# Performance work log

Hardware: AMD Instinct MI355X
Metric: run time of the kernel (lower is better)

Reference implementation:

```python
import jax, jax.numpy as jnp
import numpy as np

OUT_F, IN_F = 4096, 4096
N_FREQ = 10000
SCALING = 150.0


def iwht(x):
    """Unnormalized fast Walsh-Hadamard transform along axis 0. x: [n, m], n power of 2."""
    n, m = x.shape
    steps = int(np.log2(n))
    x = x.reshape((2,) * steps + (m,))
    for ax in range(steps):  # log2(n) butterfly stages
        a, b = jnp.split(x, 2, axis=ax)
        x = jnp.concatenate([a + b, a - b], axis=ax)
    return x.reshape(n, m)


def setup_inputs() -> dict:
    key = jax.random.key(0)
    k1, k2, k3, k4 = jax.random.split(key, 4)
    x = jax.random.normal(k1, (2, 512, IN_F), dtype=jnp.float32)
    weight = jax.random.normal(k2, (OUT_F, IN_F), dtype=jnp.float32) * 0.02
    spectrum = jax.random.normal(k3, (N_FREQ,), dtype=jnp.float32)
    indices = jax.random.randint(k4, (2, N_FREQ), 0, OUT_F, dtype=jnp.int64)
    return {"x": x, "weight": weight, "spectrum": spectrum, "indices": indices}


def reference(x, weight, spectrum, indices):
    out_f, in_f = weight.shape
    # sparse scatter of spectrum into dense (out, in) matrix
    dense = jnp.zeros((out_f, in_f), dtype=spectrum.dtype).at[indices[0], indices[1]].set(spectrum)
    # inverse WHT along out axis, scaled
    delta_w = iwht(dense) * (SCALING / np.sqrt(np.float32(out_f)))
    # F.linear(x, base_w + delta_w)
    return jnp.einsum('bsi,oi->bso', x, weight + delta_w.astype(x.dtype))
```

## Files before the change

### kernel.cpp

```cpp
#include <hip/hip_runtime.h>

typedef unsigned short ushort_t;

#define M_DIM 1024
#define N_DIM 4096
#define K_DIM 4096
#define NFREQ 10000
constexpr float SCALE = 150.0f / 64.0f;

typedef __bf16 bf16x8_t  __attribute__((ext_vector_type(8)));
typedef float  f32x16_t  __attribute__((ext_vector_type(16)));

__device__ inline ushort_t f2bf(float f) {
  union { __bf16 h; ushort_t u; } v;
  v.h = (__bf16)f;
  return v.u;
}

__global__ __launch_bounds__(256) void build_w4(
    const float* __restrict__ weight,
    const float* __restrict__ spectrum,
    const int* __restrict__ idx,
    const float* __restrict__ x,
    ushort_t* __restrict__ wb,
    ushort_t* __restrict__ xb) {
  if (blockIdx.y == 0) {
    int flat = blockIdx.x * 256 + threadIdx.x;
#pragma unroll 4
    for (int k = 0; k < 64; ++k) {
      int i = flat + k * 16384;
      float4 v = ((const float4*)x)[i];
      ushort4 o;
      o.x = f2bf(v.x); o.y = f2bf(v.y); o.z = f2bf(v.z); o.w = f2bf(v.w);
      ((ushort4*)xb)[i] = o;
    }
    return;
  }

  constexpr int CAP = 1024;
  __shared__ unsigned e_raw[CAP];
  __shared__ float    v_raw[CAP];
  __shared__ uint2    ev_srt[CAP];
  __shared__ int cnt;
  __shared__ int cstart[65];
  __shared__ int coff[64];
  __shared__ int ccnt[64];
  __shared__ unsigned walsh16[16];

  const int tid = threadIdx.x;
  const int ci0 = blockIdx.x * 64;
  const int o0  = (blockIdx.y - 1) * 256;

  if (tid == 0) cnt = 0;
  if (tid < 64) ccnt[tid] = 0;
  if (tid < 16) {
    unsigned m = tid;
    unsigned w = (m & 1 ? 0xAAAAu : 0u) ^ (m & 2 ? 0xCCCCu : 0u)
               ^ (m & 4 ? 0xF0F0u : 0u) ^ (m & 8 ? 0xFF00u : 0u);
    walsh16[m] = w;
  }
  __syncthreads();

  for (int j = tid; j < NFREQ; j += 256) {
    int c = idx[NFREQ + j];
    if ((c >> 6) == (int)blockIdx.x) {
      int p = atomicAdd(&cnt, 1);
      if (p < CAP) {
        e_raw[p] = ((unsigned)(c & 63) << 26) | ((unsigned)j << 12) | (unsigned)idx[j];
        v_raw[p] = spectrum[j];
        atomicAdd(&ccnt[c & 63], 1);
      }
    }
  }
  __syncthreads();
  const int n = cnt < CAP ? cnt : CAP;

  if (tid < 64) {
    int v = ccnt[tid];
    int s = v;
    for (int d = 1; d < 64; d <<= 1) {
      int o = __shfl_up(s, d, 64);
      if (tid >= d) s += o;
    }
    cstart[tid + 1] = s;
    if (tid == 0) cstart[0] = 0;
    coff[tid] = s - v;
  }
  __syncthreads();
  for (int e = tid; e < n; e += 256) {
    unsigned w = e_raw[e];
    int dc = w >> 26;
    int p = atomicAdd(&coff[dc], 1);
    ev_srt[p] = make_uint2(w, __float_as_uint(v_raw[e]));
  }
  __syncthreads();

  for (int e = tid; e < n; e += 256) {
    uint2 ev = ev_srt[e];
    int dc = ev.x >> 26;
    unsigned r = ev.x & 0xFFFu, j = (ev.x >> 12) & 0x3FFFu;
    int s0 = cstart[dc], e0 = cstart[dc + 1];
    bool dead = false;
    for (int p = s0; p < e0; ++p) {
      unsigned w2 = ev_srt[p].x;
      if ((w2 & 0xFFFu) == r && ((w2 >> 12) & 0x3FFFu) > j) dead = true;
    }
    if (dead) ev_srt[e].y = 0u;
  }
  __syncthreads();

  const int dc0   = (tid & 15) * 4;
  const int rof   = tid >> 4;
  const int obase = o0 + rof * 16;

  float acc[4][16];
#pragma unroll
  for (int c = 0; c < 4; ++c)
#pragma unroll
    for (int j = 0; j < 16; ++j) acc[c][j] = 0.0f;

#pragma unroll
  for (int c = 0; c < 4; ++c) {
    const int s = cstart[dc0 + c], e = cstart[dc0 + c + 1];
    for (int p = s; p < e; ++p) {
      uint2 ev = ev_srt[p];
      unsigned r = ev.x & 0xFFFu;
      unsigned W = walsh16[r & 15u];
      unsigned sx = ev.y ^ ((unsigned)(__popc(obase & r) & 1) << 31);
#pragma unroll
      for (int j = 0; j < 16; ++j) {
        acc[c][j] += __uint_as_float(sx ^ ((W << (31 - j)) & 0x80000000u));
      }
    }
  }

  size_t g = (size_t)obase * K_DIM + ci0 + dc0;
#pragma unroll
  for (int j = 0; j < 16; ++j) {
    float4 w4 = *(const float4*)&weight[g];
    ushort4 ov;
    ov.x = f2bf(w4.x + SCALE * acc[0][j]);
    ov.y = f2bf(w4.y + SCALE * acc[1][j]);
    ov.z = f2bf(w4.z + SCALE * acc[2][j]);
    ov.w = f2bf(w4.w + SCALE * acc[3][j]);
    *(ushort4*)&wb[g] = ov;
    g += K_DIM;
  }
}

__global__ __launch_bounds__(256) void gemm_bt(
    const ushort_t* __restrict__ A,
    const ushort_t* __restrict__ B,
    float* __restrict__ C0,
    float* __restrict__ C1,
    int klen) {
  constexpr int BM = 128, BN = 128, BK = 64;
  __shared__ __align__(16) ushort_t As[BM * BK];
  __shared__ __align__(16) ushort_t Bs[BN * BK];

  const int tid  = threadIdx.x;
  const int wave = tid >> 6, lane = tid & 63;
  const int wrow = wave >> 1, wcol = wave & 1;
  const int l32  = lane & 31, half = lane >> 5;

  const int fid = blockIdx.y * 32 + blockIdx.x;
  const int xcd = fid & 7, w8 = fid >> 3;
  const int sx = w8 & 7, sy = w8 >> 3;
  const int cx = xcd & 3, cy = xcd >> 2;
  const int bn = (cx * 8 + sx) * BN;
  const int bm = (cy * 4 + sy) * BM;

  const int kbeg = blockIdx.z * klen;
  float* __restrict__ dst = blockIdx.z == 0
      ? C0 : C1 + (size_t)(blockIdx.z - 1) * M_DIM * N_DIM;

  const int srow8 = lane >> 3;
  const int sq    = lane & 7;

  f32x16_t acc[2][2] = {};

  for (int kt = kbeg; kt < kbeg + klen; kt += BK) {
#pragma unroll
    for (int c = 0; c < 4; ++c) {
      int ch = wave * 4 + c;
      int gr = ch * 8 + srow8;
      int qg = sq ^ (gr & 7);
      const ushort_t* ga = A + (size_t)(bm + gr) * K_DIM + kt + qg * 8;
      __builtin_amdgcn_global_load_lds(
          (const __attribute__((address_space(1))) void*)ga,
          (__attribute__((address_space(3))) void*)&As[ch * 512], 16, 0, 0);
      const ushort_t* gb = B + (size_t)(bn + gr) * K_DIM + kt + qg * 8;
      __builtin_amdgcn_global_load_lds(
          (const __attribute__((address_space(1))) void*)gb,
          (__attribute__((address_space(3))) void*)&Bs[ch * 512], 16, 0, 0);
    }
    __syncthreads();

    bf16x8_t af[2][4], bfr[2][4];
#pragma unroll
    for (int mi = 0; mi < 2; ++mi) {
#pragma unroll
      for (int h = 0; h < 4; ++h) {
        int q = h * 2 + half;
        int ar = wrow * 64 + mi * 32 + l32;
        af[mi][h]  = *(const bf16x8_t*)&As[ar * BK + ((q ^ (ar & 7)) * 8)];
        int br = wcol * 64 + mi * 32 + l32;
        bfr[mi][h] = *(const bf16x8_t*)&Bs[br * BK + ((q ^ (br & 7)) * 8)];
      }
    }
#pragma unroll
    for (int h = 0; h < 4; ++h)
#pragma unroll
      for (int mi = 0; mi < 2; ++mi)
#pragma unroll
        for (int nj = 0; nj < 2; ++nj)
          acc[mi][nj] = __builtin_amdgcn_mfma_f32_32x32x16_bf16(
              af[mi][h], bfr[nj][h], acc[mi][nj], 0, 0, 0);
    __syncthreads();
  }

#pragma unroll
  for (int mi = 0; mi < 2; ++mi) {
#pragma unroll
    for (int nj = 0; nj < 2; ++nj) {
      int col  = bn + wcol * 64 + nj * 32 + l32;
      int rwb  = bm + wrow * 64 + mi * 32 + 4 * half;
#pragma unroll
      for (int reg = 0; reg < 16; ++reg) {
        int row = rwb + (reg & 3) + 8 * (reg >> 2);
        dst[(size_t)row * N_DIM + col] = acc[mi][nj][reg];
      }
    }
  }
}

__global__ __launch_bounds__(256) void reduce_n(float* __restrict__ out,
                                                const float* __restrict__ part,
                                                int npart) {
  int i = blockIdx.x * 256 + threadIdx.x;
  float4 a = ((const float4*)out)[i];
  for (int t = 0; t < npart; ++t) {
    float4 b = ((const float4*)(part + (size_t)t * M_DIM * N_DIM))[i];
    a.x += b.x; a.y += b.y; a.z += b.z; a.w += b.w;
  }
  ((float4*)out)[i] = a;
}

extern "C" void kernel_launch(void* const* d_in, const int* in_sizes, int n_in,
                              void* d_out, int out_size, void* d_ws, size_t ws_size,
                              hipStream_t stream) {
  const float* x        = (const float*)d_in[0];
  const float* weight   = (const float*)d_in[1];
  const float* spectrum = (const float*)d_in[2];
  const int*   indices  = (const int*)d_in[3];
  float* out = (float*)d_out;

  char* ws = (char*)d_ws;
  const size_t WB_BYTES = (size_t)N_DIM * K_DIM * 2;
  const size_t XB_BYTES = (size_t)M_DIM * K_DIM * 2;
  const size_t P1_BYTES = (size_t)M_DIM * N_DIM * 4;

  ushort_t* wb = (ushort_t*)ws;
  ushort_t* xb = (ushort_t*)(ws + WB_BYTES);
  float* part = (float*)(ws + WB_BYTES + XB_BYTES);

  int zsplit = (ws_size >= WB_BYTES + XB_BYTES + P1_BYTES) ? 2 : 1;

  build_w4<<<dim3(64, 17), 256, 0, stream>>>(weight, spectrum, indices, x, wb, xb);

  gemm_bt<<<dim3(N_DIM / 128, M_DIM / 128, zsplit), 256, 0, stream>>>(
      xb, wb, out, part, K_DIM / zsplit);
  if (zsplit > 1)
    reduce_n<<<(M_DIM * N_DIM / 4) / 256, 256, 0, stream>>>(out, part, zsplit - 1);
}
```

Before: 185.8 us.

## Triple-buffer GEMM LDS loads with async prefetch and larger 128x256 tiles

Replaces the single-buffered bf16 GEMM with a 3-stage LDS pipeline. Global-to-LDS loads for tile t+2 are issued while tile t is computed, and the per-tile syncthreads pairs become a vmcnt wait plus one barrier. The block tile grows to 128x256 with 512 threads (8 waves), the XCD-aware tile mapping is adjusted, and MFMA sections get raised wave priority. This aims to hide global load latency behind MFMA work. The cost is much more LDS per block (144KB), which limits occupancy, and fewer blocks (128 per z-slice) on a large CU count.

```diff
diff --git a/kernel.cpp b/kernel.cpp
--- a/kernel.cpp
+++ b/kernel.cpp
@@ -148,66 +148,101 @@
   }
 }
 
-__global__ __launch_bounds__(256) void gemm_bt(
+__global__ __launch_bounds__(512) void gemm_pipe(
     const ushort_t* __restrict__ A,
     const ushort_t* __restrict__ B,
     float* __restrict__ C0,
     float* __restrict__ C1,
     int klen) {
-  constexpr int BM = 128, BN = 128, BK = 64;
-  __shared__ __align__(16) ushort_t As[BM * BK];
-  __shared__ __align__(16) ushort_t Bs[BN * BK];
+  constexpr int BM = 128, BN = 256, BK = 64;
+  constexpr int A_US = BM * BK;
+  constexpr int B_US = BN * BK;
+  __shared__ __align__(16) ushort_t lds[3 * (A_US + B_US)];
 
   const int tid  = threadIdx.x;
   const int wave = tid >> 6, lane = tid & 63;
-  const int wrow = wave >> 1, wcol = wave & 1;
+  const int wrow = wave >> 2;
+  const int wcol = wave & 3;
   const int l32  = lane & 31, half = lane >> 5;
 
-  const int fid = blockIdx.y * 32 + blockIdx.x;
-  const int xcd = fid & 7, w8 = fid >> 3;
-  const int sx = w8 & 7, sy = w8 >> 3;
-  const int cx = xcd & 3, cy = xcd >> 2;
-  const int bn = (cx * 8 + sx) * BN;
-  const int bm = (cy * 4 + sy) * BM;
+  const int fid = blockIdx.y * 16 + blockIdx.x;
+  const int xcd = fid & 7, w16 = fid >> 3;
+  const int bn = ((xcd & 3) * 4 + (w16 & 3)) * BN;
+  const int bm = ((xcd >> 2) * 4 + (w16 >> 2)) * BM;
 
   const int kbeg = blockIdx.z * klen;
+  const int nt   = klen / BK;
   float* __restrict__ dst = blockIdx.z == 0
       ? C0 : C1 + (size_t)(blockIdx.z - 1) * M_DIM * N_DIM;
 
-  const int srow8 = lane >> 3;
-  const int sq    = lane & 7;
+  auto stage = [&](int tt, int p) {
+    const int kt = kbeg + tt * BK;
+    ushort_t* abase = lds + p * A_US;
+    ushort_t* bbase = lds + 3 * A_US + p * B_US;
+#pragma unroll
+    for (int l = 0; l < 6; ++l) {
+      int s  = tid + l * 512;
+      int sb = (tid & ~63) + l * 512;
+      if (l < 2) {
+        int gr = s >> 3, qg = (s & 7) ^ (gr & 7);
+        const ushort_t* ga = A + (size_t)(bm + gr) * K_DIM + kt + qg * 8;
+        __builtin_amdgcn_global_load_lds(
+            (const __attribute__((address_space(1))) void*)ga,
+            (__attribute__((address_space(3))) void*)(abase + sb * 8), 16, 0, 0);
+      } else {
+        int s2 = s - 1024;
+        int gr = s2 >> 3, qg = (s2 & 7) ^ (gr & 7);
+        const ushort_t* gb = B + (size_t)(bn + gr) * K_DIM + kt + qg * 8;
+        __builtin_amdgcn_global_load_lds(
+            (const __attribute__((address_space(1))) void*)gb,
+            (__attribute__((address_space(3))) void*)(bbase + (sb - 1024) * 8), 16, 0, 0);
+      }
+    }
+  };
 
   f32x16_t acc[2][2] = {};
 
-  for (int kt = kbeg; kt < kbeg + klen; kt += BK) {
-#pragma unroll
-    for (int c = 0; c < 4; ++c) {
-      int ch = wave * 4 + c;
-      int gr = ch * 8 + srow8;
-      int qg = sq ^ (gr & 7);
-      const ushort_t* ga = A + (size_t)(bm + gr) * K_DIM + kt + qg * 8;
-      __builtin_amdgcn_global_load_lds(
-          (const __attribute__((address_space(1))) void*)ga,
-          (__attribute__((address_space(3))) void*)&As[ch * 512], 16, 0, 0);
-      const ushort_t* gb = B + (size_t)(bn + gr) * K_DIM + kt + qg * 8;
-      __builtin_amdgcn_global_load_lds(
-          (const __attribute__((address_space(1))) void*)gb,
-          (__attribute__((address_space(3))) void*)&Bs[ch * 512], 16, 0, 0);
-    }
-    __syncthreads();
+  stage(0, 0);
+  if (nt > 1) {
+    stage(1, 1);
+    __builtin_amdgcn_sched_barrier(0);
+    asm volatile("s_waitcnt vmcnt(6)" ::: "memory");
+  } else {
+    __builtin_amdgcn_sched_barrier(0);
+    asm volatile("s_waitcnt vmcnt(0)" ::: "memory");
+  }
+  __builtin_amdgcn_sched_barrier(0);
+  __builtin_amdgcn_s_barrier();
+  __builtin_amdgcn_sched_barrier(0);
+
+  for (int t = 0; t < nt; ++t) {
+    const int cb = t % 3;
+    const ushort_t* as_ = lds + cb * A_US;
+    const ushort_t* bs_ = lds + 3 * A_US + cb * B_US;
+
+    if (t + 2 < nt) stage(t + 2, (t + 2) % 3);
 
     bf16x8_t af[2][4], bfr[2][4];
 #pragma unroll
     for (int mi = 0; mi < 2; ++mi) {
+      int ar = wrow * 64 + mi * 32 + l32;
 #pragma unroll
       for (int h = 0; h < 4; ++h) {
         int q = h * 2 + half;
-        int ar = wrow * 64 + mi * 32 + l32;
-        af[mi][h]  = *(const bf16x8_t*)&As[ar * BK + ((q ^ (ar & 7)) * 8)];
-        int br = wcol * 64 + mi * 32 + l32;
-        bfr[mi][h] = *(const bf16x8_t*)&Bs[br * BK + ((q ^ (br & 7)) * 8)];
-      }
-    }
+        af[mi][h] = *(const bf16x8_t*)&as_[ar * BK + ((q ^ (ar & 7)) * 8)];
+      }
+    }
+#pragma unroll
+    for (int nj = 0; nj < 2; ++nj) {
+      int br = wcol * 64 + nj * 32 + l32;
+#pragma unroll
+      for (int h = 0; h < 4; ++h) {
+        int q = h * 2 + half;
+        bfr[nj][h] = *(const bf16x8_t*)&bs_[br * BK + ((q ^ (br & 7)) * 8)];
+      }
+    }
+
+    __builtin_amdgcn_s_setprio(1);
 #pragma unroll
     for (int h = 0; h < 4; ++h)
 #pragma unroll
@@ -216,7 +251,21 @@
         for (int nj = 0; nj < 2; ++nj)
           acc[mi][nj] = __builtin_amdgcn_mfma_f32_32x32x16_bf16(
               af[mi][h], bfr[nj][h], acc[mi][nj], 0, 0, 0);
-    __syncthreads();
+    __builtin_amdgcn_s_setprio(0);
+
+    if (t + 2 < nt) {
+      __builtin_amdgcn_sched_barrier(0);
+      asm volatile("s_waitcnt vmcnt(6)" ::: "memory");
+      __builtin_amdgcn_sched_barrier(0);
+      __builtin_amdgcn_s_barrier();
+      __builtin_amdgcn_sched_barrier(0);
+    } else if (t + 1 < nt) {
+      __builtin_amdgcn_sched_barrier(0);
+      asm volatile("s_waitcnt vmcnt(0)" ::: "memory");
+      __builtin_amdgcn_sched_barrier(0);
+      __builtin_amdgcn_s_barrier();
+      __builtin_amdgcn_sched_barrier(0);
+    }
   }
 
 #pragma unroll
@@ -268,7 +317,7 @@
 
   build_w4<<<dim3(64, 17), 256, 0, stream>>>(weight, spectrum, indices, x, wb, xb);
 
-  gemm_bt<<<dim3(N_DIM / 128, M_DIM / 128, zsplit), 256, 0, stream>>>(
+  gemm_pipe<<<dim3(N_DIM / 256, M_DIM / 128, zsplit), 512, 0, stream>>>(
       xb, wb, out, part, K_DIM / zsplit);
   if (zsplit > 1)
     reduce_n<<<(M_DIM * N_DIM / 4) / 256, 256, 0, stream>>>(out, part, zsplit - 1);
```

Measured after the change: 186.4 us. No clear change (+0.3%).

## Fuse split-K reduction into GEMM epilogue via per-tile tickets and ready flags

Applied to the files above, without the earlier changes.

Drops the separate reduce kernel. Each output tile's two split-K blocks take a ticket. The first writes its partial to the workspace and raises a ready flag, and the second spins on that flag and writes the summed result to out. Build_w4 resets the flags each launch. This removes a kernel launch and one full read-modify-write pass over out, at the cost of a spin-wait. The spin-wait can deadlock if the second-arriving block is resident while its partner is not scheduled, and it can stall waves.

```diff
diff --git a/kernel.cpp b/kernel.cpp
--- a/kernel.cpp
+++ b/kernel.cpp
@@ -23,9 +23,17 @@
     const int* __restrict__ idx,
     const float* __restrict__ x,
     ushort_t* __restrict__ wb,
-    ushort_t* __restrict__ xb) {
+    ushort_t* __restrict__ xb,
+    int* __restrict__ tickets,
+    int* __restrict__ ready) {
   if (blockIdx.y == 0) {
     int flat = blockIdx.x * 256 + threadIdx.x;
+    if (blockIdx.x == 0) {
+      __hip_atomic_store(&tickets[threadIdx.x], 0,
+                         __ATOMIC_RELAXED, __HIP_MEMORY_SCOPE_AGENT);
+      __hip_atomic_store(&ready[threadIdx.x], 0,
+                         __ATOMIC_RELAXED, __HIP_MEMORY_SCOPE_AGENT);
+    }
 #pragma unroll 4
     for (int k = 0; k < 64; ++k) {
       int i = flat + k * 16384;
@@ -151,12 +159,15 @@
 __global__ __launch_bounds__(256) void gemm_bt(
     const ushort_t* __restrict__ A,
     const ushort_t* __restrict__ B,
-    float* __restrict__ C0,
-    float* __restrict__ C1,
+    float* __restrict__ out,
+    float* __restrict__ part,
+    int* __restrict__ tickets,
+    int* __restrict__ ready,
     int klen) {
   constexpr int BM = 128, BN = 128, BK = 64;
   __shared__ __align__(16) ushort_t As[BM * BK];
   __shared__ __align__(16) ushort_t Bs[BN * BK];
+  __shared__ int tkt_s;
 
   const int tid  = threadIdx.x;
   const int wave = tid >> 6, lane = tid & 63;
@@ -171,8 +182,6 @@
   const int bm = (cy * 4 + sy) * BM;
 
   const int kbeg = blockIdx.z * klen;
-  float* __restrict__ dst = blockIdx.z == 0
-      ? C0 : C1 + (size_t)(blockIdx.z - 1) * M_DIM * N_DIM;
 
   const int srow8 = lane >> 3;
   const int sq    = lane & 7;
@@ -219,31 +228,65 @@
     __syncthreads();
   }
 
-#pragma unroll
-  for (int mi = 0; mi < 2; ++mi) {
-#pragma unroll
-    for (int nj = 0; nj < 2; ++nj) {
-      int col  = bn + wcol * 64 + nj * 32 + l32;
-      int rwb  = bm + wrow * 64 + mi * 32 + 4 * half;
-#pragma unroll
-      for (int reg = 0; reg < 16; ++reg) {
-        int row = rwb + (reg & 3) + 8 * (reg >> 2);
-        dst[(size_t)row * N_DIM + col] = acc[mi][nj][reg];
-      }
-    }
-  }
-}
-
-__global__ __launch_bounds__(256) void reduce_n(float* __restrict__ out,
-                                                const float* __restrict__ part,
-                                                int npart) {
-  int i = blockIdx.x * 256 + threadIdx.x;
-  float4 a = ((const float4*)out)[i];
-  for (int t = 0; t < npart; ++t) {
-    float4 b = ((const float4*)(part + (size_t)t * M_DIM * N_DIM))[i];
-    a.x += b.x; a.y += b.y; a.z += b.z; a.w += b.w;
-  }
-  ((float4*)out)[i] = a;
+  if (gridDim.z == 1) {
+#pragma unroll
+    for (int mi = 0; mi < 2; ++mi)
+#pragma unroll
+      for (int nj = 0; nj < 2; ++nj) {
+        int col  = bn + wcol * 64 + nj * 32 + l32;
+        int rwb  = bm + wrow * 64 + mi * 32 + 4 * half;
+#pragma unroll
+        for (int reg = 0; reg < 16; ++reg) {
+          int row = rwb + (reg & 3) + 8 * (reg >> 2);
+          out[(size_t)row * N_DIM + col] = acc[mi][nj][reg];
+        }
+      }
+    return;
+  }
+
+  if (tid == 0) tkt_s = atomicAdd(&tickets[fid], 1);
+  __syncthreads();
+  const bool first = (tkt_s == 0);
+
+  if (first) {
+#pragma unroll
+    for (int mi = 0; mi < 2; ++mi)
+#pragma unroll
+      for (int nj = 0; nj < 2; ++nj) {
+        int col  = bn + wcol * 64 + nj * 32 + l32;
+        int rwb  = bm + wrow * 64 + mi * 32 + 4 * half;
+#pragma unroll
+        for (int reg = 0; reg < 16; ++reg) {
+          int row = rwb + (reg & 3) + 8 * (reg >> 2);
+          part[(size_t)row * N_DIM + col] = acc[mi][nj][reg];
+        }
+      }
+    __threadfence();
+    __syncthreads();
+    if (tid == 0)
+      __hip_atomic_store(&ready[fid], 1, __ATOMIC_RELEASE,
+                         __HIP_MEMORY_SCOPE_AGENT);
+  } else {
+    if (tid == 0) {
+      while (__hip_atomic_load(&ready[fid], __ATOMIC_ACQUIRE,
+                               __HIP_MEMORY_SCOPE_AGENT) == 0)
+        __builtin_amdgcn_s_sleep(1);
+    }
+    __syncthreads();
+#pragma unroll
+    for (int mi = 0; mi < 2; ++mi)
+#pragma unroll
+      for (int nj = 0; nj < 2; ++nj) {
+        int col  = bn + wcol * 64 + nj * 32 + l32;
+        int rwb  = bm + wrow * 64 + mi * 32 + 4 * half;
+#pragma unroll
+        for (int reg = 0; reg < 16; ++reg) {
+          int row = rwb + (reg & 3) + 8 * (reg >> 2);
+          size_t o = (size_t)row * N_DIM + col;
+          out[o] = part[o] + acc[mi][nj][reg];
+        }
+      }
+  }
 }
 
 extern "C" void kernel_launch(void* const* d_in, const int* in_sizes, int n_in,
@@ -259,17 +302,20 @@
   const size_t WB_BYTES = (size_t)N_DIM * K_DIM * 2;
   const size_t XB_BYTES = (size_t)M_DIM * K_DIM * 2;
   const size_t P1_BYTES = (size_t)M_DIM * N_DIM * 4;
+  const size_t FLAG_BYTES = 2 * 256 * sizeof(int);
 
   ushort_t* wb = (ushort_t*)ws;
   ushort_t* xb = (ushort_t*)(ws + WB_BYTES);
-  float* part = (float*)(ws + WB_BYTES + XB_BYTES);
-
-  int zsplit = (ws_size >= WB_BYTES + XB_BYTES + P1_BYTES) ? 2 : 1;
-
-  build_w4<<<dim3(64, 17), 256, 0, stream>>>(weight, spectrum, indices, x, wb, xb);
+  float* part  = (float*)(ws + WB_BYTES + XB_BYTES);
+  int* tickets = (int*)(ws + WB_BYTES + XB_BYTES + P1_BYTES);
+  int* ready   = tickets + 256;
+
+  int zsplit =
+      (ws_size >= WB_BYTES + XB_BYTES + P1_BYTES + FLAG_BYTES) ? 2 : 1;
+
+  build_w4<<<dim3(64, 17), 256, 0, stream>>>(weight, spectrum, indices, x,
+                                             wb, xb, tickets, ready);
 
   gemm_bt<<<dim3(N_DIM / 128, M_DIM / 128, zsplit), 256, 0, stream>>>(
-      xb, wb, out, part, K_DIM / zsplit);
-  if (zsplit > 1)
-    reduce_n<<<(M_DIM * N_DIM / 4) / 256, 256, 0, stream>>>(out, part, zsplit - 1);
+      xb, wb, out, part, tickets, ready, K_DIM / zsplit);
 }
```

Result: slower. 222.3 us (+19.6%).

## Apply sparse Walsh delta to activations instead of materializing dense delta weight

Applied to the files above, without the earlier changes.

Instead of building W + iWHT(delta) densely, the weight is just converted to bf16, and the sparse spectrum contribution is applied per output row: each block scatters spectrum*x into a 4096-vector in shared memory and runs an in-LDS Walsh-Hadamard transform, then adds it to the GEMM result. The split-K reduction is fused into this step. It removes the dense per-element Walsh accumulation from weight building, at the cost of 1024 blocks each doing an LDS WHT and shared-memory atomics, and it keeps the delta in fp32 instead of rounding it into bf16 weights.

```diff
diff --git a/kernel.cpp b/kernel.cpp
--- a/kernel.cpp
+++ b/kernel.cpp
@@ -17,26 +17,15 @@
   return v.u;
 }
 
-__global__ __launch_bounds__(256) void build_w4(
+__global__ __launch_bounds__(256) void prep_cvt(
     const float* __restrict__ weight,
+    const float* __restrict__ x,
     const float* __restrict__ spectrum,
     const int* __restrict__ idx,
-    const float* __restrict__ x,
-    ushort_t* __restrict__ wb,
-    ushort_t* __restrict__ xb) {
-  if (blockIdx.y == 0) {
-    int flat = blockIdx.x * 256 + threadIdx.x;
-#pragma unroll 4
-    for (int k = 0; k < 64; ++k) {
-      int i = flat + k * 16384;
-      float4 v = ((const float4*)x)[i];
-      ushort4 o;
-      o.x = f2bf(v.x); o.y = f2bf(v.y); o.z = f2bf(v.z); o.w = f2bf(v.w);
-      ((ushort4*)xb)[i] = o;
-    }
-    return;
-  }
-
+    ushort_t* __restrict__ wbb,
+    ushort_t* __restrict__ xb,
+    uint2* __restrict__ ent,
+    int* __restrict__ cst) {
   constexpr int CAP = 1024;
   __shared__ unsigned e_raw[CAP];
   __shared__ float    v_raw[CAP];
@@ -45,25 +34,38 @@
   __shared__ int cstart[65];
   __shared__ int coff[64];
   __shared__ int ccnt[64];
-  __shared__ unsigned walsh16[16];
 
   const int tid = threadIdx.x;
-  const int ci0 = blockIdx.x * 64;
-  const int o0  = (blockIdx.y - 1) * 256;
-
+
+  if (blockIdx.x >= 64) {
+    const int i0 = (blockIdx.x - 64) * 256 + tid;
+#pragma unroll
+    for (int k = 0; k < 8; ++k) {
+      int i = i0 + k * 524288;
+      float4 v = ((const float4*)weight)[i];
+      ushort4 o;
+      o.x = f2bf(v.x); o.y = f2bf(v.y); o.z = f2bf(v.z); o.w = f2bf(v.w);
+      ((ushort4*)wbb)[i] = o;
+    }
+#pragma unroll
+    for (int k = 0; k < 2; ++k) {
+      int i = i0 + k * 524288;
+      float4 v = ((const float4*)x)[i];
+      ushort4 o;
+      o.x = f2bf(v.x); o.y = f2bf(v.y); o.z = f2bf(v.z); o.w = f2bf(v.w);
+      ((ushort4*)xb)[i] = o;
+    }
+    return;
+  }
+
+  const int g = blockIdx.x;
   if (tid == 0) cnt = 0;
   if (tid < 64) ccnt[tid] = 0;
-  if (tid < 16) {
-    unsigned m = tid;
-    unsigned w = (m & 1 ? 0xAAAAu : 0u) ^ (m & 2 ? 0xCCCCu : 0u)
-               ^ (m & 4 ? 0xF0F0u : 0u) ^ (m & 8 ? 0xFF00u : 0u);
-    walsh16[m] = w;
-  }
   __syncthreads();
 
   for (int j = tid; j < NFREQ; j += 256) {
     int c = idx[NFREQ + j];
-    if ((c >> 6) == (int)blockIdx.x) {
+    if ((c >> 6) == g) {
       int p = atomicAdd(&cnt, 1);
       if (p < CAP) {
         e_raw[p] = ((unsigned)(c & 63) << 26) | ((unsigned)j << 12) | (unsigned)idx[j];
@@ -109,43 +111,8 @@
   }
   __syncthreads();
 
-  const int dc0   = (tid & 15) * 4;
-  const int rof   = tid >> 4;
-  const int obase = o0 + rof * 16;
-
-  float acc[4][16];
-#pragma unroll
-  for (int c = 0; c < 4; ++c)
-#pragma unroll
-    for (int j = 0; j < 16; ++j) acc[c][j] = 0.0f;
-
-#pragma unroll
-  for (int c = 0; c < 4; ++c) {
-    const int s = cstart[dc0 + c], e = cstart[dc0 + c + 1];
-    for (int p = s; p < e; ++p) {
-      uint2 ev = ev_srt[p];
-      unsigned r = ev.x & 0xFFFu;
-      unsigned W = walsh16[r & 15u];
-      unsigned sx = ev.y ^ ((unsigned)(__popc(obase & r) & 1) << 31);
-#pragma unroll
-      for (int j = 0; j < 16; ++j) {
-        acc[c][j] += __uint_as_float(sx ^ ((W << (31 - j)) & 0x80000000u));
-      }
-    }
-  }
-
-  size_t g = (size_t)obase * K_DIM + ci0 + dc0;
-#pragma unroll
-  for (int j = 0; j < 16; ++j) {
-    float4 w4 = *(const float4*)&weight[g];
-    ushort4 ov;
-    ov.x = f2bf(w4.x + SCALE * acc[0][j]);
-    ov.y = f2bf(w4.y + SCALE * acc[1][j]);
-    ov.z = f2bf(w4.z + SCALE * acc[2][j]);
-    ov.w = f2bf(w4.w + SCALE * acc[3][j]);
-    *(ushort4*)&wb[g] = ov;
-    g += K_DIM;
-  }
+  for (int e = tid; e < n; e += 256) ent[g * CAP + e] = ev_srt[e];
+  if (tid < 65) cst[g * 72 + tid] = cstart[tid];
 }
 
 __global__ __launch_bounds__(256) void gemm_bt(
@@ -234,16 +201,69 @@
   }
 }
 
-__global__ __launch_bounds__(256) void reduce_n(float* __restrict__ out,
-                                                const float* __restrict__ part,
-                                                int npart) {
-  int i = blockIdx.x * 256 + threadIdx.x;
-  float4 a = ((const float4*)out)[i];
-  for (int t = 0; t < npart; ++t) {
-    float4 b = ((const float4*)(part + (size_t)t * M_DIM * N_DIM))[i];
-    a.x += b.x; a.y += b.y; a.z += b.z; a.w += b.w;
-  }
-  ((float4*)out)[i] = a;
+__global__ __launch_bounds__(256) void delta_fuse(
+    const float* __restrict__ x,
+    float* __restrict__ out,
+    const float* __restrict__ part,
+    const uint2* __restrict__ ent,
+    const int* __restrict__ cst,
+    int npart) {
+  __shared__ float xrow[4096];
+  __shared__ float D[4096];
+  const int tid = threadIdx.x;
+  const int m = blockIdx.x;
+
+  const float* xr = x + (size_t)m * K_DIM;
+#pragma unroll
+  for (int i = 0; i < 4; ++i) {
+    int t = tid + i * 256;
+    float4 v = ((const float4*)xr)[t];
+    *(float4*)&xrow[t * 4] = v;
+    *(float4*)&D[t * 4] = make_float4(0.f, 0.f, 0.f, 0.f);
+  }
+  __syncthreads();
+
+  for (int g = 0; g < 64; ++g) {
+    const int n = cst[g * 72 + 64];
+    for (int e = tid; e < n; e += 256) {
+      uint2 ev = ent[g * 1024 + e];
+      int dc = ev.x >> 26;
+      int r  = ev.x & 0xFFFu;
+      float v = __uint_as_float(ev.y);
+      atomicAdd(&D[r], v * xrow[g * 64 + dc]);
+    }
+  }
+  __syncthreads();
+
+  for (int s = 0; s < 12; ++s) {
+    const int str = 1 << s;
+#pragma unroll
+    for (int t8 = 0; t8 < 8; ++t8) {
+      int t  = tid + t8 * 256;
+      int lo = (t & (str - 1)) | ((t & ~(str - 1)) << 1);
+      float a = D[lo], b = D[lo + str];
+      D[lo] = a + b;
+      D[lo + str] = a - b;
+    }
+    __syncthreads();
+  }
+
+  float* orow = out + (size_t)m * N_DIM;
+  const float* prow = part + (size_t)m * N_DIM;
+#pragma unroll
+  for (int i = 0; i < 4; ++i) {
+    int base = (tid + i * 256) * 4;
+    float4 o = *(const float4*)&orow[base];
+    if (npart) {
+      float4 p = *(const float4*)&prow[base];
+      o.x += p.x; o.y += p.y; o.z += p.z; o.w += p.w;
+    }
+    o.x += SCALE * D[base + 0];
+    o.y += SCALE * D[base + 1];
+    o.z += SCALE * D[base + 2];
+    o.w += SCALE * D[base + 3];
+    *(float4*)&orow[base] = o;
+  }
 }
 
 extern "C" void kernel_launch(void* const* d_in, const int* in_sizes, int n_in,
@@ -256,20 +276,26 @@
   float* out = (float*)d_out;
 
   char* ws = (char*)d_ws;
-  const size_t WB_BYTES = (size_t)N_DIM * K_DIM * 2;
-  const size_t XB_BYTES = (size_t)M_DIM * K_DIM * 2;
-  const size_t P1_BYTES = (size_t)M_DIM * N_DIM * 4;
-
-  ushort_t* wb = (ushort_t*)ws;
-  ushort_t* xb = (ushort_t*)(ws + WB_BYTES);
-  float* part = (float*)(ws + WB_BYTES + XB_BYTES);
-
-  int zsplit = (ws_size >= WB_BYTES + XB_BYTES + P1_BYTES) ? 2 : 1;
-
-  build_w4<<<dim3(64, 17), 256, 0, stream>>>(weight, spectrum, indices, x, wb, xb);
+  const size_t WB_BYTES  = (size_t)N_DIM * K_DIM * 2;
+  const size_t XB_BYTES  = (size_t)M_DIM * K_DIM * 2;
+  const size_t ENT_BYTES = (size_t)64 * 1024 * sizeof(uint2);
+  const size_t CST_BYTES = (size_t)64 * 72 * sizeof(int);
+  const size_t P1_BYTES  = (size_t)M_DIM * N_DIM * 4;
+
+  ushort_t* wbb = (ushort_t*)ws;
+  ushort_t* xb  = (ushort_t*)(ws + WB_BYTES);
+  uint2* ent    = (uint2*)(ws + WB_BYTES + XB_BYTES);
+  int*   cst    = (int*)(ws + WB_BYTES + XB_BYTES + ENT_BYTES);
+  float* part   = (float*)(ws + WB_BYTES + XB_BYTES + ENT_BYTES + CST_BYTES);
+
+  int zsplit = (ws_size >= WB_BYTES + XB_BYTES + ENT_BYTES + CST_BYTES +
+                P1_BYTES) ? 2 : 1;
+
+  prep_cvt<<<64 + 2048, 256, 0, stream>>>(weight, x, spectrum, indices,
+                                          wbb, xb, ent, cst);
 
   gemm_bt<<<dim3(N_DIM / 128, M_DIM / 128, zsplit), 256, 0, stream>>>(
-      xb, wb, out, part, K_DIM / zsplit);
-  if (zsplit > 1)
-    reduce_n<<<(M_DIM * N_DIM / 4) / 256, 256, 0, stream>>>(out, part, zsplit - 1);
-}
+      xb, wbb, out, part, K_DIM / zsplit);
+
+  delta_fuse<<<M_DIM, 256, 0, stream>>>(x, out, part, ent, cst, zsplit - 1);
+}
```

After: 243.8 us. 31.2% more time.
